# Performance work log

Measured on AMD Instinct MI355X. Metric: run time of the kernel, lower is better.

The kernel has to match this reference:

```python
import jax, jax.numpy as jnp
import numpy as np

DIM = 256
HEADS = 8
NX = NY = 48
RNG = 5
MAX_IDX = (RNG + 1) ** 2  # 36, padding token


def _make_tokens(nx, ny, rng):
    # Half-symmetric tokenization of 2D relative positions (Learnable_rel_pos_embedding.tokenize)
    xm, ym = np.meshgrid(np.arange(nx), np.arange(ny), indexing='ij')
    xm, ym = xm.ravel(), ym.ravel()
    dx = xm[None, :] - xm[:, None]
    dy = ym[None, :] - ym[:, None]
    tok = np.abs(dx) * (rng + 1) + np.abs(dy)
    tok[(np.abs(dx) > rng) | (np.abs(dy) > rng)] = MAX_IDX
    return tok.astype(np.int32)


def setup_inputs() -> dict:
    key = jax.random.key(0)
    ks = jax.random.split(key, 10)
    s = DIM ** -0.5
    x = jax.random.normal(ks[0], (1, DIM, NX, NY), dtype=jnp.float32)
    Wq = jax.random.normal(ks[1], (DIM, DIM), dtype=jnp.float32) * s
    bq = jax.random.normal(ks[2], (DIM,), dtype=jnp.float32) * 0.01
    Wk = jax.random.normal(ks[3], (DIM, DIM), dtype=jnp.float32) * s
    bk = jax.random.normal(ks[4], (DIM,), dtype=jnp.float32) * 0.01
    Wv = jax.random.normal(ks[5], (DIM, DIM), dtype=jnp.float32) * s
    bv = jax.random.normal(ks[6], (DIM,), dtype=jnp.float32) * 0.01
    Wp = jax.random.normal(ks[7], (DIM, DIM), dtype=jnp.float32) * s
    bp = jax.random.normal(ks[8], (DIM,), dtype=jnp.float32) * 0.01
    emb = jax.random.normal(ks[9], (MAX_IDX + 1, HEADS), dtype=jnp.float32) * 0.02
    tokens = jnp.asarray(_make_tokens(NX, NY, RNG))  # (N, N) int32
    return dict(x=x, Wq=Wq, bq=bq, Wk=Wk, bk=bk, Wv=Wv, bv=bv,
                Wp=Wp, bp=bp, emb=emb, tokens=tokens)


def reference(x, Wq, bq, Wk, bk, Wv, bv, Wp, bp, emb, tokens):
    B, C, nx, ny = x.shape
    H = emb.shape[1]
    hd = C // H
    N = nx * ny
    scale = hd ** -0.5

    def conv1x1(W, b, t):
        return (jnp.einsum('oc,bcxy->boxy', W, t) + b[None, :, None, None])

    # Q/K/V as 1x1 convs, split into heads: (B, H, hd, N)
    q = conv1x1(Wq, bq, x).reshape(B, H, hd, N)
    k = conv1x1(Wk, bk, x).reshape(B, H, hd, N)
    v = conv1x1(Wv, bv, x).reshape(B, H, hd, N)

    # attn_method=2: scores = scale*QK^T + relative positional bias
    scores = jnp.einsum('bhdn,bhdm->bhnm', q, k) * scale  # (B, H, N, N)

    # pos_type=5: embedding lookup over half-symmetric relative-position tokens
    pad = emb.shape[0] - 1
    emb_masked = emb.at[pad].set(0.0)  # padding_idx row is zero
    pe = emb_masked[tokens]            # (N, N, H)
    scores = scores + jnp.transpose(pe, (2, 0, 1))[None]

    attn = jax.nn.softmax(scores, axis=-1)
    out = jnp.einsum('bhnm,bhdm->bhdn', attn, v).reshape(B, C, nx, ny)
    out = conv1x1(Wp, bp, out)
    return out
```

## Files before the change

kernel.cpp:

```cpp
#include <hip/hip_runtime.h>

#define NN 2304
#define CC 256
#define HH 8
#define HD 32
#define NYY 48
#define SCALE 0.17677669529663687f

typedef __bf16 bf16_t;
typedef __bf16 bf8v __attribute__((ext_vector_type(8)));
typedef float f4v __attribute__((ext_vector_type(4)));

__device__ __forceinline__ f4v mfma16(bf8v a, bf8v b, f4v c) {
    return __builtin_amdgcn_mfma_f32_16x16x32_bf16(a, b, c, 0, 0, 0);
}

__device__ __forceinline__ bf8v cvt_w8(const float* p) {
    float4 a = *(const float4*)p;
    float4 c = *(const float4*)(p + 4);
    bf8v o;
    o[0] = (bf16_t)a.x; o[1] = (bf16_t)a.y; o[2] = (bf16_t)a.z; o[3] = (bf16_t)a.w;
    o[4] = (bf16_t)c.x; o[5] = (bf16_t)c.y; o[6] = (bf16_t)c.z; o[7] = (bf16_t)c.w;
    return o;
}

__global__ __launch_bounds__(256) void k_proj_qkv(
    const float* __restrict__ Wq, const float* __restrict__ Wk,
    const float* __restrict__ Wv,
    const float* __restrict__ bq, const float* __restrict__ bk,
    const float* __restrict__ bv,
    const float* __restrict__ x,
    bf16_t* __restrict__ Qt, bf16_t* __restrict__ Kt, bf16_t* __restrict__ Vd) {
    const int mat = blockIdx.z;
    const float* Wf = (mat == 0) ? Wq : (mat == 1) ? Wk : Wv;
    const float* bias = (mat == 0) ? bq : (mat == 1) ? bk : bv;
    const int n0 = blockIdx.x * 32;
    const int o0 = blockIdx.y * 64;
    const int t = threadIdx.x;
    const int lane = t & 63;
    const int wave = t >> 6;
    const int l15 = lane & 15;
    const int quad = lane >> 4;
    const int orow = o0 + wave * 16;

    __shared__ bf16_t xs[32][256];
    {
        const int sn = t & 31;
        const int scg = t >> 5;
#pragma unroll
        for (int i = 0; i < 4; i++) {
            const int cb = i * 8 + scg;
            const int c0s = cb * 8;
            bf8v o;
#pragma unroll
            for (int j = 0; j < 8; j++) {
                o[j] = (bf16_t)x[(size_t)(c0s + j) * NN + n0 + sn];
            }
            *(bf8v*)(&xs[sn][(cb ^ (sn & 7)) * 8]) = o;
        }
    }
    __syncthreads();

    f4v acc0 = {0.f, 0.f, 0.f, 0.f}, acc1 = {0.f, 0.f, 0.f, 0.f};
#pragma unroll
    for (int k0 = 0; k0 < CC; k0 += 32) {
        bf8v af = cvt_w8(Wf + (size_t)(orow + l15) * CC + k0 + quad * 8);
        const int pcb = ((k0 >> 3) + quad);
        bf8v b0 = *(const bf8v*)(&xs[l15][(pcb ^ (l15 & 7)) * 8]);
        bf8v b1 = *(const bf8v*)(&xs[16 + l15][(pcb ^ (l15 & 7)) * 8]);
        acc0 = mfma16(af, b0, acc0);
        acc1 = mfma16(af, b1, acc1);
    }

#pragma unroll
    for (int r = 0; r < 4; r++) {
        const int o = orow + quad * 4 + r;
        const float bo = bias[o];
#pragma unroll
        for (int nb = 0; nb < 2; nb++) {
            const int n = n0 + nb * 16 + l15;
            float v = (nb ? acc1[r] : acc0[r]) + bo;
            if (mat == 2) {
                Vd[(size_t)o * NN + n] = (bf16_t)v;
            } else {
                int h = o >> 5, d = o & 31;
                bf16_t* dst = (mat == 0) ? Qt : Kt;
                float vv = (mat == 0) ? v * SCALE : v;
                dst[(size_t)h * NN * HD + (size_t)n * HD + d] = (bf16_t)vv;
            }
        }
    }
}

__global__ __launch_bounds__(256, 4) void k_attn(
    const bf16_t* __restrict__ Qt, const bf16_t* __restrict__ Kt,
    const bf16_t* __restrict__ Vd, const float* __restrict__ emb,
    bf16_t* __restrict__ Yt) {
    __shared__ float lds_emb[40];
    __shared__ float red[4][16][33];
    __shared__ float reds[4][16];
    __shared__ bf16_t lds_p[4][16 * 32];
    const int b = blockIdx.x;
    const int h = b & 7;
    const int qt = b >> 3;
    const int t = threadIdx.x;
    if (t < 37) lds_emb[t] = (t < 36) ? emb[t * HH + h] : 0.0f;
    __syncthreads();

    const int wave = t >> 6, lane = t & 63;
    const int l15 = lane & 15, quad = lane >> 4;
    const int qg0 = qt * 16;
    const bf16_t* Qh = Qt + (size_t)h * NN * HD;
    const bf16_t* Kh = Kt + (size_t)h * NN * HD;
    const bf16_t* Vh = Vd + (size_t)h * HD * NN;

    const bf8v aq = *(const bf8v*)(Qh + (size_t)(qg0 + l15) * HD + quad * 8);

    int xi[4], yi[4];
#pragma unroll
    for (int r = 0; r < 4; r++) {
        int qi = qg0 + quad * 4 + r;
        xi[r] = qi / NYY;
        yi[r] = qi - xi[r] * NYY;
    }
    const int xi_lo = qg0 / NYY;
    const int xi_hi = (qg0 + 15) / NYY;

    f4v o0 = {0.f, 0.f, 0.f, 0.f}, o1 = {0.f, 0.f, 0.f, 0.f};
    const f4v z = {0.f, 0.f, 0.f, 0.f};
    float lsum[4] = {0.f, 0.f, 0.f, 0.f};
    bf16_t* plds = &lds_p[wave][0];

    const int k_begin = wave * (NN / 4), k_end = k_begin + NN / 4;
    for (int kb = k_begin; kb < k_end; kb += 32) {
        bf8v kf0 = *(const bf8v*)(Kh + (size_t)(kb + l15) * HD + quad * 8);
        bf8v kf1 = *(const bf8v*)(Kh + (size_t)(kb + 16 + l15) * HD + quad * 8);
        bf8v vf0 = *(const bf8v*)(Vh + (size_t)l15 * NN + kb + quad * 8);
        bf8v vf1 = *(const bf8v*)(Vh + (size_t)(16 + l15) * NN + kb + quad * 8);
        f4v s0 = mfma16(aq, kf0, z);
        f4v s1 = mfma16(aq, kf1, z);

        const int xj_lo = kb / NYY;
        const int xj_hi = (kb + 31) / NYY;
        if (xj_lo > xi_hi + 5 || xj_hi + 5 < xi_lo) {
#pragma unroll
            for (int cb = 0; cb < 2; cb++) {
                const f4v& s = cb ? s1 : s0;
#pragma unroll
                for (int r = 0; r < 4; r++) {
                    float p = __expf(s[r]);
                    lsum[r] += p;
                    plds[(quad * 4 + r) * 32 + cb * 16 + l15] = (bf16_t)p;
                }
            }
        } else {
#pragma unroll
            for (int cb = 0; cb < 2; cb++) {
                const f4v& s = cb ? s1 : s0;
                int kj = kb + cb * 16 + l15;
                int xj = kj / NYY;
                int yj = kj - xj * NYY;
#pragma unroll
                for (int r = 0; r < 4; r++) {
                    int dx = xi[r] - xj; dx = dx < 0 ? -dx : dx;
                    int dy = yi[r] - yj; dy = dy < 0 ? -dy : dy;
                    int tok = (dx > 5 || dy > 5) ? 36 : dx * 6 + dy;
                    float p = __expf(s[r] + lds_emb[tok]);
                    lsum[r] += p;
                    plds[(quad * 4 + r) * 32 + cb * 16 + l15] = (bf16_t)p;
                }
            }
        }
        bf8v ap = *(const bf8v*)(plds + l15 * 32 + quad * 8);
        o0 = mfma16(ap, vf0, o0);
        o1 = mfma16(ap, vf1, o1);
    }

#pragma unroll
    for (int r = 0; r < 4; r++) {
        float v = lsum[r];
#pragma unroll
        for (int m = 1; m < 16; m <<= 1) v += __shfl_xor(v, m, 64);
        const int row = quad * 4 + r;
        red[wave][row][l15] = o0[r];
        red[wave][row][16 + l15] = o1[r];
        if (l15 == 0) reds[wave][row] = v;
    }
    __syncthreads();

#pragma unroll
    for (int e = t; e < 512; e += 256) {
        const int row = e >> 5;
        const int d = e & 31;
        float so = red[0][row][d] + red[1][row][d] + red[2][row][d] + red[3][row][d];
        float sl = reds[0][row] + reds[1][row] + reds[2][row] + reds[3][row];
        Yt[(size_t)(qg0 + row) * CC + h * HD + d] = (bf16_t)(so / sl);
    }
}

__global__ __launch_bounds__(256) void k_proj_out(
    const float* __restrict__ Wp, const float* __restrict__ bp,
    const bf16_t* __restrict__ Yt, float* __restrict__ out) {
    const int n0 = blockIdx.x * 32;
    const int o0 = blockIdx.y * 64;
    const int lane = threadIdx.x & 63;
    const int wave = threadIdx.x >> 6;
    const int l15 = lane & 15;
    const int quad = lane >> 4;
    const int orow = o0 + wave * 16;

    f4v acc0 = {0.f, 0.f, 0.f, 0.f}, acc1 = {0.f, 0.f, 0.f, 0.f};
#pragma unroll
    for (int k0 = 0; k0 < CC; k0 += 32) {
        bf8v af = cvt_w8(Wp + (size_t)(orow + l15) * CC + k0 + quad * 8);
        bf8v b0 = *(const bf8v*)(Yt + (size_t)(n0 + l15) * CC + k0 + quad * 8);
        bf8v b1 = *(const bf8v*)(Yt + (size_t)(n0 + 16 + l15) * CC + k0 + quad * 8);
        acc0 = mfma16(af, b0, acc0);
        acc1 = mfma16(af, b1, acc1);
    }

#pragma unroll
    for (int r = 0; r < 4; r++) {
        const int o = orow + quad * 4 + r;
        const float bo = bp[o];
        out[(size_t)o * NN + n0 + l15] = acc0[r] + bo;
        out[(size_t)o * NN + n0 + 16 + l15] = acc1[r] + bo;
    }
}

extern "C" void kernel_launch(void* const* d_in, const int* in_sizes, int n_in,
                              void* d_out, int out_size, void* d_ws, size_t ws_size,
                              hipStream_t stream) {
    const float* x   = (const float*)d_in[0];
    const float* Wq  = (const float*)d_in[1];
    const float* bq  = (const float*)d_in[2];
    const float* Wk  = (const float*)d_in[3];
    const float* bk  = (const float*)d_in[4];
    const float* Wv  = (const float*)d_in[5];
    const float* bv  = (const float*)d_in[6];
    const float* Wp  = (const float*)d_in[7];
    const float* bp  = (const float*)d_in[8];
    const float* emb = (const float*)d_in[9];
    float* out = (float*)d_out;

    bf16_t* Qt = (bf16_t*)d_ws;
    bf16_t* Kt = Qt + (size_t)NN * CC;
    bf16_t* Vd = Kt + (size_t)NN * CC;
    bf16_t* Yt = Vd + (size_t)NN * CC;

    hipLaunchKernelGGL(k_proj_qkv, dim3(72, 4, 3), dim3(256), 0, stream,
                       Wq, Wk, Wv, bq, bk, bv, x, Qt, Kt, Vd);
    hipLaunchKernelGGL(k_attn, dim3(1152), dim3(256), 0, stream,
                       Qt, Kt, Vd, emb, Yt);
    hipLaunchKernelGGL(k_proj_out, dim3(72, 4), dim3(256), 0, stream, Wp, bp, Yt, out);
}
```

Measured before the change: 140.6 us.

## Transpose score MFMA and pass P via cross-lane shuffles instead of LDS

New measurement: 144.7 us. 2.9% more time.

```diff
diff --git a/kernel.cpp b/kernel.cpp
--- a/kernel.cpp
+++ b/kernel.cpp
@@ -10,6 +10,7 @@
 typedef __bf16 bf16_t;
 typedef __bf16 bf8v __attribute__((ext_vector_type(8)));
 typedef float f4v __attribute__((ext_vector_type(4)));
+typedef unsigned int u32x4 __attribute__((ext_vector_type(4)));
 
 __device__ __forceinline__ f4v mfma16(bf8v a, bf8v b, f4v c) {
     return __builtin_amdgcn_mfma_f32_16x16x32_bf16(a, b, c, 0, 0, 0);
@@ -22,6 +23,12 @@
     o[0] = (bf16_t)a.x; o[1] = (bf16_t)a.y; o[2] = (bf16_t)a.z; o[3] = (bf16_t)a.w;
     o[4] = (bf16_t)c.x; o[5] = (bf16_t)c.y; o[6] = (bf16_t)c.z; o[7] = (bf16_t)c.w;
     return o;
+}
+
+__device__ __forceinline__ unsigned int pk2(float a, float b) {
+    unsigned short lo = __builtin_bit_cast(unsigned short, (bf16_t)a);
+    unsigned short hi = __builtin_bit_cast(unsigned short, (bf16_t)b);
+    return ((unsigned int)hi << 16) | lo;
 }
 
 __global__ __launch_bounds__(256) void k_proj_qkv(
@@ -99,7 +106,6 @@
     __shared__ float lds_emb[40];
     __shared__ float red[4][16][33];
     __shared__ float reds[4][16];
-    __shared__ bf16_t lds_p[4][16 * 32];
     const int b = blockIdx.x;
     const int h = b & 7;
     const int qt = b >> 3;
@@ -116,20 +122,18 @@
 
     const bf8v aq = *(const bf8v*)(Qh + (size_t)(qg0 + l15) * HD + quad * 8);
 
-    int xi[4], yi[4];
-#pragma unroll
-    for (int r = 0; r < 4; r++) {
-        int qi = qg0 + quad * 4 + r;
-        xi[r] = qi / NYY;
-        yi[r] = qi - xi[r] * NYY;
-    }
+    const int qi = qg0 + l15;
+    const int xiq = qi / NYY;
+    const int yiq = qi - xiq * NYY;
     const int xi_lo = qg0 / NYY;
     const int xi_hi = (qg0 + 15) / NYY;
 
     f4v o0 = {0.f, 0.f, 0.f, 0.f}, o1 = {0.f, 0.f, 0.f, 0.f};
     const f4v z = {0.f, 0.f, 0.f, 0.f};
-    float lsum[4] = {0.f, 0.f, 0.f, 0.f};
-    bf16_t* plds = &lds_p[wave][0];
+    float lsum = 0.f;
+    const bool lowq = (quad & 1) == 0;
+    const bool lowpair = quad < 2;
+    const bool keepown = (quad == 0) || (quad == 3);
 
     const int k_begin = wave * (NN / 4), k_end = k_begin + NN / 4;
     for (int kb = k_begin; kb < k_end; kb += 32) {
@@ -137,55 +141,76 @@
         bf8v kf1 = *(const bf8v*)(Kh + (size_t)(kb + 16 + l15) * HD + quad * 8);
         bf8v vf0 = *(const bf8v*)(Vh + (size_t)l15 * NN + kb + quad * 8);
         bf8v vf1 = *(const bf8v*)(Vh + (size_t)(16 + l15) * NN + kb + quad * 8);
-        f4v s0 = mfma16(aq, kf0, z);
-        f4v s1 = mfma16(aq, kf1, z);
-
+        f4v s0 = mfma16(kf0, aq, z);
+        f4v s1 = mfma16(kf1, aq, z);
+
+        float p[8];
         const int xj_lo = kb / NYY;
         const int xj_hi = (kb + 31) / NYY;
         if (xj_lo > xi_hi + 5 || xj_hi + 5 < xi_lo) {
 #pragma unroll
-            for (int cb = 0; cb < 2; cb++) {
-                const f4v& s = cb ? s1 : s0;
-#pragma unroll
-                for (int r = 0; r < 4; r++) {
-                    float p = __expf(s[r]);
-                    lsum[r] += p;
-                    plds[(quad * 4 + r) * 32 + cb * 16 + l15] = (bf16_t)p;
-                }
+            for (int r = 0; r < 4; r++) {
+                p[r] = __expf(s0[r]);
+                p[4 + r] = __expf(s1[r]);
             }
         } else {
 #pragma unroll
-            for (int cb = 0; cb < 2; cb++) {
-                const f4v& s = cb ? s1 : s0;
-                int kj = kb + cb * 16 + l15;
+            for (int r = 0; r < 4; r++) {
+                int kj = kb + quad * 4 + r;
                 int xj = kj / NYY;
                 int yj = kj - xj * NYY;
-#pragma unroll
-                for (int r = 0; r < 4; r++) {
-                    int dx = xi[r] - xj; dx = dx < 0 ? -dx : dx;
-                    int dy = yi[r] - yj; dy = dy < 0 ? -dy : dy;
-                    int tok = (dx > 5 || dy > 5) ? 36 : dx * 6 + dy;
-                    float p = __expf(s[r] + lds_emb[tok]);
-                    lsum[r] += p;
-                    plds[(quad * 4 + r) * 32 + cb * 16 + l15] = (bf16_t)p;
-                }
+                int dx = xiq - xj; dx = dx < 0 ? -dx : dx;
+                int dy = yiq - yj; dy = dy < 0 ? -dy : dy;
+                int tok = (dx > 5 || dy > 5) ? 36 : dx * 6 + dy;
+                p[r] = __expf(s0[r] + lds_emb[tok]);
+                int kj2 = kj + 16;
+                int xj2 = kj2 / NYY;
+                int yj2 = kj2 - xj2 * NYY;
+                int dx2 = xiq - xj2; dx2 = dx2 < 0 ? -dx2 : dx2;
+                int dy2 = yiq - yj2; dy2 = dy2 < 0 ? -dy2 : dy2;
+                int tok2 = (dx2 > 5 || dy2 > 5) ? 36 : dx2 * 6 + dy2;
+                p[4 + r] = __expf(s1[r] + lds_emb[tok2]);
             }
         }
-        bf8v ap = *(const bf8v*)(plds + l15 * 32 + quad * 8);
-        o0 = mfma16(ap, vf0, o0);
-        o1 = mfma16(ap, vf1, o1);
-    }
+        lsum += p[0] + p[1] + p[2] + p[3] + p[4] + p[5] + p[6] + p[7];
+
+        unsigned int pk0 = pk2(p[0], p[1]);
+        unsigned int pk1 = pk2(p[2], p[3]);
+        unsigned int pk2_ = pk2(p[4], p[5]);
+        unsigned int pk3 = pk2(p[6], p[7]);
+        unsigned int x0 = __shfl_xor((int)pk0, 16);
+        unsigned int x1 = __shfl_xor((int)pk1, 16);
+        unsigned int x2 = __shfl_xor((int)pk2_, 16);
+        unsigned int x3 = __shfl_xor((int)pk3, 16);
+        unsigned int S0_0 = lowq ? pk0 : x0, S0_1 = lowq ? pk1 : x1;
+        unsigned int S0_2 = lowq ? x0 : pk0, S0_3 = lowq ? x1 : pk1;
+        unsigned int S1_0 = lowq ? pk2_ : x2, S1_1 = lowq ? pk3 : x3;
+        unsigned int S1_2 = lowq ? x2 : pk2_, S1_3 = lowq ? x3 : pk3;
+        unsigned int r0 = __shfl_xor((int)(lowpair ? S1_0 : S0_0), 32);
+        unsigned int r1 = __shfl_xor((int)(lowpair ? S1_1 : S0_1), 32);
+        unsigned int r2 = __shfl_xor((int)(lowpair ? S1_2 : S0_2), 32);
+        unsigned int r3 = __shfl_xor((int)(lowpair ? S1_3 : S0_3), 32);
+        u32x4 Bv;
+        Bv.x = keepown ? (lowpair ? S0_0 : S1_0) : r0;
+        Bv.y = keepown ? (lowpair ? S0_1 : S1_1) : r1;
+        Bv.z = keepown ? (lowpair ? S0_2 : S1_2) : r2;
+        Bv.w = keepown ? (lowpair ? S0_3 : S1_3) : r3;
+        bf8v pb = __builtin_bit_cast(bf8v, Bv);
+
+        o0 = mfma16(vf0, pb, o0);
+        o1 = mfma16(vf1, pb, o1);
+    }
+
+    float v = lsum;
+    v += __shfl_xor(v, 16);
+    v += __shfl_xor(v, 32);
 
 #pragma unroll
     for (int r = 0; r < 4; r++) {
-        float v = lsum[r];
-#pragma unroll
-        for (int m = 1; m < 16; m <<= 1) v += __shfl_xor(v, m, 64);
-        const int row = quad * 4 + r;
-        red[wave][row][l15] = o0[r];
-        red[wave][row][16 + l15] = o1[r];
-        if (l15 == 0) reds[wave][row] = v;
-    }
+        red[wave][l15][quad * 4 + r] = o0[r];
+        red[wave][l15][16 + quad * 4 + r] = o1[r];
+    }
+    if (lane < 16) reds[wave][lane] = v;
     __syncthreads();
 
 #pragma unroll
```
